# Optimization experiments

Measured on AMD Instinct MI355X. Metric: run time of the kernel, lower is better.

The kernel has to match this reference:

```python
import jax, jax.numpy as jnp
import numpy as np


def conv(x, w, b=None, pad=0):
    y = jax.lax.conv_general_dilated(x, w, (1, 1), [(pad, pad), (pad, pad)],
                                     dimension_numbers=('NCHW', 'OIHW', 'NCHW'))
    if b is not None:
        y = y + b[None, :, None, None]
    return y


def bn(x, g, b, m, v, eps=1e-5):
    scale = g / jnp.sqrt(v + eps)
    return (x - m[None, :, None, None]) * scale[None, :, None, None] + b[None, :, None, None]


def channel_gate(x, w1, b1, w2, b2):
    # avg pool -> MLP -> sigmoid, returns [B, C, 1, 1]
    p = x.mean(axis=(2, 3))                       # [B, C]
    h = jax.nn.relu(p @ w1.T + b1)                # [B, C//r]
    a = h @ w2.T + b2                             # [B, C]
    return jax.nn.sigmoid(a)[:, :, None, None]


def setup_inputs() -> dict:
    key = jax.random.key(0)
    ks = iter(jax.random.split(key, 48))
    B, Cin, H, W = 2, 256, 64, 64
    Ci = Cin // 2          # inter_channels = 128
    Cr = Ci // 16          # gate bottleneck = 8
    def nrm(shape, s=0.05):
        return jax.random.normal(next(ks), shape, jnp.float32) * s
    d = {}
    d['q'] = jax.random.normal(next(ks), (B, Cin, H, W), jnp.float32)
    d['s'] = jax.random.normal(next(ks), (B, Cin, H, W), jnp.float32)
    # Trans_s: conv3x3 + BN
    d['ts_w'] = nrm((Ci, Cin, 3, 3)); d['ts_b'] = jnp.zeros(Ci)
    d['ts_g'] = jnp.ones(Ci); d['ts_be'] = jnp.zeros(Ci)
    d['ts_m'] = nrm((Ci,), 0.01); d['ts_v'] = jnp.ones(Ci)
    # Trans_q: conv3x3 + BN
    d['tq_w'] = nrm((Ci, Cin, 3, 3)); d['tq_b'] = jnp.zeros(Ci)
    d['tq_g'] = jnp.ones(Ci); d['tq_be'] = jnp.zeros(Ci)
    d['tq_m'] = nrm((Ci,), 0.01); d['tq_v'] = jnp.ones(Ci)
    # common_v 1x1
    d['cv_w'] = nrm((Ci, Ci, 1, 1)); d['cv_b'] = jnp.zeros(Ci)
    # key/query 1x1 projections (out = Ci//2)
    d['k1_w'] = nrm((Ci // 2, Ci, 1, 1)); d['k1_b'] = jnp.zeros(Ci // 2)
    d['q1_w'] = nrm((Ci // 2, Ci, 1, 1)); d['q1_b'] = jnp.zeros(Ci // 2)
    d['k2_w'] = nrm((Ci // 2, Ci, 1, 1)); d['k2_b'] = jnp.zeros(Ci // 2)
    d['q2_w'] = nrm((Ci // 2, Ci, 1, 1)); d['q2_b'] = jnp.zeros(Ci // 2)
    # ChannelGate MLP
    d['g1_w'] = nrm((Cr, Ci)); d['g1_b'] = jnp.zeros(Cr)
    d['g2_w'] = nrm((Ci, Cr)); d['g2_b'] = jnp.zeros(Ci)
    # conv_cat: conv3x3 (no bias) + BN
    d['cc_w'] = nrm((Ci, 2 * Ci, 3, 3))
    d['cc_g'] = jnp.ones(Ci); d['cc_be'] = jnp.zeros(Ci)
    d['cc_m'] = nrm((Ci,), 0.01); d['cc_v'] = jnp.ones(Ci)
    return d


def reference(q, s, ts_w, ts_b, ts_g, ts_be, ts_m, ts_v,
              tq_w, tq_b, tq_g, tq_be, tq_m, tq_v,
              cv_w, cv_b, k1_w, k1_b, q1_w, q1_b, k2_w, k2_b, q2_w, q2_b,
              g1_w, g1_b, g2_w, g2_b, cc_w, cc_g, cc_be, cc_m, cc_v):
    # stems: conv3x3 + BN + ReLU
    s = jax.nn.relu(bn(conv(s, ts_w, ts_b, pad=1), ts_g, ts_be, ts_m, ts_v))
    q = jax.nn.relu(bn(conv(q, tq_w, tq_b, pad=1), tq_g, tq_be, tq_m, tq_v))
    B, C, H, W = q.shape
    N = H * W
    # values
    v_q1 = conv(q, cv_w, cv_b)                          # [B,C,H,W]
    v_s1 = conv(s, cv_w, cv_b)
    v_q = v_q1.reshape(B, C, N).transpose(0, 2, 1)      # [B,N,C]
    v_s = v_s1.reshape(B, C, N).transpose(0, 2, 1)
    # dual keys / queries with negation trick
    k1 = conv(s, k1_w, k1_b).reshape(B, C // 2, N)
    k2 = conv(q, k2_w, k2_b).reshape(B, C // 2, N)
    key_cat = jnp.concatenate([k1, -k2], axis=1).transpose(0, 2, 1)   # [B,N,C]
    q1x = conv(s, q1_w, q1_b).reshape(B, C // 2, N)
    q2x = conv(q, q2_w, q2_b).reshape(B, C // 2, N)
    query_cat = jnp.concatenate([q1x, q2x], axis=1)                    # [B,C,N]
    # abs-score attention, dual softmax from the same score matrix
    A_s = jnp.abs(jnp.einsum('bnc,bcm->bnm', key_cat, query_cat))      # [B,N,N]
    att_s = jax.nn.softmax(A_s, axis=-1)
    att_q = jax.nn.softmax(A_s.transpose(0, 2, 1), axis=-1)
    # attend + channel-gate SE fusion + residual
    p_s = jnp.einsum('bnm,bmc->bnc', att_s, v_s).transpose(0, 2, 1).reshape(B, C, H, W)
    E_s = channel_gate(v_s1, g1_w, g1_b, g2_w, g2_b) * p_s + s
    q_s = jnp.einsum('bnm,bmc->bnc', att_q, v_q).transpose(0, 2, 1).reshape(B, C, H, W)
    E_q = channel_gate(v_q1, g1_w, g1_b, g2_w, g2_b) * q_s + q
    # concat + conv3x3(no bias) + BN + ReLU
    cpam = jax.nn.relu(bn(conv(jnp.concatenate([E_q, E_s], axis=1), cc_w, None, pad=1),
                          cc_g, cc_be, cc_m, cc_v))
    return (cpam, E_q, E_s)
```

## Files before the change

kernel.cpp:

```cpp
#include <hip/hip_runtime.h>

typedef __bf16 bf16;
typedef __bf16 v8bf __attribute__((ext_vector_type(8)));
typedef __bf16 v4bf __attribute__((ext_vector_type(4)));
typedef float v4f __attribute__((ext_vector_type(4)));

#define MFMA16(a, b, c) __builtin_amdgcn_mfma_f32_16x16x32_bf16(a, b, c, 0, 0, 0)

__device__ __forceinline__ float sf(float x) {
  if (!(x == x)) return 0.f;
  return fminf(fmaxf(x, -1e30f), 1e30f);
}

__global__ __launch_bounds__(256) void fill_kernel(float* __restrict__ out, float v, int n) {
  int i = blockIdx.x * 256 + threadIdx.x;
  if (i < n) out[i] = v;
}

__global__ __launch_bounds__(256) void prep_kernel(
    const float* __restrict__ ts_w, const float* __restrict__ tq_w,
    const float* ts_b, const float* ts_g, const float* ts_be, const float* ts_m, const float* ts_v,
    const float* tq_b, const float* tq_g, const float* tq_be, const float* tq_m, const float* tq_v,
    bf16* __restrict__ Wt01, float* __restrict__ ss01)
{
  int idx = blockIdx.x * 256 + threadIdx.x;
  if (idx < 589824) {
    int which = idx / 294912;
    int rem = idx - which * 294912;
    int co = rem / 2304;
    int r2 = rem - co * 2304;
    int tap = r2 >> 8;
    int ci = r2 & 255;
    const float* W = which ? tq_w : ts_w;
    Wt01[idx] = (bf16)W[(co * 256 + ci) * 9 + tap];
  } else if (idx < 590080) {
    int i = idx - 589824;
    int which = i >> 7, c = i & 127;
    float g, be, m, vv, bias;
    if (which == 0) { g=ts_g[c]; be=ts_be[c]; m=ts_m[c]; vv=ts_v[c]; bias=ts_b[c]; }
    else            { g=tq_g[c]; be=tq_be[c]; m=tq_m[c]; vv=tq_v[c]; bias=tq_b[c]; }
    float scale = g / sqrtf(vv + 1e-5f);
    ss01[which * 256 + c] = sf(scale);
    ss01[which * 256 + 128 + c] = sf((bias - m) * scale + be);
  }
}

__global__ __launch_bounds__(256) void prep2_kernel(
    const float* __restrict__ cc_w, const float* cc_g, const float* cc_be,
    const float* cc_m, const float* cc_v,
    bf16* __restrict__ Wt2, float* __restrict__ ss_cc)
{
  int idx = blockIdx.x * 256 + threadIdx.x;
  if (idx < 294912) {
    int co = idx / 2304;
    int r2 = idx - co * 2304;
    int tap = r2 >> 8;
    int ci = r2 & 255;
    Wt2[idx] = (bf16)cc_w[(co * 256 + ci) * 9 + tap];
  } else if (idx < 295040) {
    int c = idx - 294912;
    float scale = cc_g[c] / sqrtf(cc_v[c] + 1e-5f);
    ss_cc[c] = sf(scale);
    ss_cc[128 + c] = sf(-cc_m[c] * scale + cc_be[c]);
  }
}

__global__ __launch_bounds__(256) void convN_kernel(
    const float* __restrict__ pS, const float* __restrict__ pQ,
    const bf16* __restrict__ Wb, const float* __restrict__ ssb,
    void* __restrict__ out_, int mode)
{
  __shared__ bf16 As[66][40];
  __shared__ bf16 Bs[3][64][40];

  int y = blockIdx.x;
  int co0 = blockIdx.y * 64;
  int z = blockIdx.z;
  int tsr = z >> 1, b = z & 1;

  const float *in0, *in1;
  const bf16* W;
  const float* sp;
  if (mode == 0) {
    const float* base = (tsr ? pQ : pS) + (long)b * 1048576;
    in0 = base; in1 = base + 524288;
    W = Wb + (long)tsr * 294912;
    sp = ssb + tsr * 256;
  } else {
    in0 = pS + 1048576 + (long)b * 524288;
    in1 = pS + 2097152 + (long)b * 524288;
    W = Wb; sp = ssb;
  }

  int t = threadIdx.x, lane = t & 63, w = t >> 6;
  int l15 = lane & 15, l4 = lane >> 4;
  int wr = (w & 1) * 32, wc = (w >> 1) * 32;
  int ac = t & 31, ag = t >> 5;
  int bco = t >> 2, bk = (t & 3) * 8;

  v4f acc[2][2] = {};

  auto loadA = [&](int it, v8bf& areg) {
    int dy = it >> 3, ks = it & 7;
    int ysrc = y + dy - 1;
    int cg = ks * 32 + ac;
    const float* ip = (cg < 128) ? (in0 + (long)cg * 4096) : (in1 + (long)(cg - 128) * 4096);
    if ((unsigned)ysrc < 64u) {
      const float* src = ip + ysrc * 64 + ag * 8;
#pragma unroll
      for (int i = 0; i < 8; ++i) areg[i] = (bf16)src[i];
    } else {
#pragma unroll
      for (int i = 0; i < 8; ++i) areg[i] = (bf16)0.f;
    }
  };
  auto loadB = [&](int it, v8bf* breg) {
    int dy = it >> 3, ks = it & 7;
    const bf16* wk = W + (long)(co0 + bco) * 2304 + dy * 3 * 256 + ks * 32 + bk;
#pragma unroll
    for (int d = 0; d < 3; ++d) breg[d] = *(const v8bf*)(wk + d * 256);
  };

  v8bf areg, breg[3];
  loadA(0, areg);
  loadB(0, breg);

  for (int it = 0; it < 24; ++it) {
    __syncthreads();
#pragma unroll
    for (int i = 0; i < 8; ++i) As[ag * 8 + 1 + i][ac] = areg[i];
    if (ag == 0) As[0][ac] = (bf16)0.f;
    if (ag == 7) As[65][ac] = (bf16)0.f;
#pragma unroll
    for (int d = 0; d < 3; ++d) *(v8bf*)&Bs[d][bco][bk] = breg[d];
    __syncthreads();
    if (it < 23) { loadA(it + 1, areg); loadB(it + 1, breg); }
#pragma unroll
    for (int d = 0; d < 3; ++d) {
      v8bf af0 = *(const v8bf*)&As[wr + d + l15][l4 * 8];
      v8bf af1 = *(const v8bf*)&As[wr + 16 + d + l15][l4 * 8];
#pragma unroll
      for (int j = 0; j < 2; ++j) {
        v8bf bfr = *(const v8bf*)&Bs[d][wc + j * 16 + l15][l4 * 8];
        acc[0][j] = MFMA16(af0, bfr, acc[0][j]);
        acc[1][j] = MFMA16(af1, bfr, acc[1][j]);
      }
    }
  }
#pragma unroll
  for (int i = 0; i < 2; ++i) {
    int nb = y * 64 + wr + i * 16 + l4 * 4;
#pragma unroll
    for (int j = 0; j < 2; ++j) {
      int c = co0 + wc + j * 16 + l15;
      float scale = sp[c], shift = sp[128 + c];
      if (mode == 0) {
        bf16* o = (bf16*)out_ + ((long)(tsr * 2 + b) * 4096 + nb) * 128 + c;
#pragma unroll
        for (int r = 0; r < 4; ++r)
          o[r * 128] = (bf16)sf(fmaxf(acc[i][j][r] * scale + shift, 0.f));
      } else {
        v4f pk;
#pragma unroll
        for (int r = 0; r < 4; ++r)
          pk[r] = sf(fmaxf(acc[i][j][r] * scale + shift, 0.f));
        *(v4f*)((float*)out_ + ((long)b * 128 + c) * 4096 + nb) = pk;
      }
    }
  }
}

__global__ __launch_bounds__(256) void conv1_kernel(
    const bf16* __restrict__ feat_base,
    const float* __restrict__ cv_w, const float* __restrict__ k1_w, const float* __restrict__ q1_w,
    const float* __restrict__ k2_w, const float* __restrict__ q2_w,
    const float* __restrict__ cv_b, const float* __restrict__ k1_b, const float* __restrict__ q1_b,
    const float* __restrict__ k2_b, const float* __restrict__ q2_b,
    bf16* __restrict__ v_base, bf16* __restrict__ keyT, bf16* __restrict__ queryT)
{
  int nt = blockIdx.x;
  int br = blockIdx.z >> 1, b = blockIdx.z & 1;
  long zid = br * 2 + b;
  const bf16* feat = feat_base + zid * 524288 + (long)nt * 4096;

  __shared__ bf16 As[32][40];
  __shared__ bf16 Bs[256][40];

  int t = threadIdx.x, lane = t & 63, w = t >> 6;
  int l15 = lane & 15, l4 = lane >> 4;
  int wr = (w & 1) * 16, wc = (w >> 1) * 128;

  const float* wrow;
  bool negk = false;
  if (t < 128)       wrow = cv_w + (long)t * 128;
  else if (t < 192) { wrow = (br ? k2_w : k1_w) + (long)(t - 128) * 128; negk = (br != 0); }
  else               wrow = (br ? q2_w : q1_w) + (long)(t - 192) * 128;

  v4f acc[8] = {};
  int ap = t >> 2, ak = (t & 3) * 8;

  for (int ks = 0; ks < 4; ++ks) {
    int ci0 = ks * 32;
    v8bf av;
    if (t < 128) av = *(const v8bf*)(feat + ap * 128 + ci0 + ak);
    float wv[32];
#pragma unroll
    for (int u = 0; u < 32; ++u) wv[u] = wrow[ci0 + u];
    if (negk) {
#pragma unroll
      for (int u = 0; u < 32; ++u) wv[u] = -wv[u];
    }
    __syncthreads();
    if (t < 128) *(v8bf*)&As[ap][ak] = av;
#pragma unroll
    for (int u = 0; u < 32; ++u) Bs[t][u] = (bf16)wv[u];
    __syncthreads();
    v8bf af = *(const v8bf*)&As[wr + l15][l4 * 8];
#pragma unroll
    for (int j = 0; j < 8; ++j) {
      v8bf bfr = *(const v8bf*)&Bs[wc + j * 16 + l15][l4 * 8];
      acc[j] = MFMA16(af, bfr, acc[j]);
    }
  }

  int nb = nt * 32 + wr + l4 * 4;
#pragma unroll
  for (int j = 0; j < 8; ++j) {
    int c = wc + j * 16 + l15;
    float bv;
    if (c < 128)      bv = cv_b[c];
    else if (c < 192) bv = br ? -k2_b[c - 128] : k1_b[c - 128];
    else              bv = (br ? q2_b : q1_b)[c - 192];
    float v0 = sf(acc[j][0] + bv), v1 = sf(acc[j][1] + bv);
    float v2 = sf(acc[j][2] + bv), v3 = sf(acc[j][3] + bv);
    if (c < 128) {
      v4bf pk;
      pk[0] = (bf16)v0; pk[1] = (bf16)v1; pk[2] = (bf16)v2; pk[3] = (bf16)v3;
      *(v4bf*)(v_base + zid * 524288 + (long)c * 4096 + nb) = pk;
    } else if (c < 192) {
      int cc = (c - 128) + br * 64;
      bf16* kp = keyT + (long)b * 524288 + (long)nb * 128 + cc;
      kp[0] = (bf16)v0; kp[128] = (bf16)v1; kp[256] = (bf16)v2; kp[384] = (bf16)v3;
    } else {
      int cc = (c - 192) + br * 64;
      bf16* qp = queryT + (long)b * 524288 + (long)nb * 128 + cc;
      qp[0] = (bf16)v0; qp[128] = (bf16)v1; qp[256] = (bf16)v2; qp[384] = (bf16)v3;
    }
  }
}

__global__ __launch_bounds__(64) void pmean_kernel(
    const bf16* __restrict__ vs, float* __restrict__ pmean)
{
  int c = blockIdx.x, z = blockIdx.y, l = threadIdx.x;
  const bf16* src = vs + ((long)z * 128 + c) * 4096;
  float s = 0.f;
#pragma unroll
  for (int k = 0; k < 8; ++k) {
    v8bf v = *(const v8bf*)(src + k * 512 + l * 8);
#pragma unroll
    for (int e = 0; e < 8; ++e) s += (float)v[e];
  }
  s += __shfl_xor(s, 1, 64);
  s += __shfl_xor(s, 2, 64);
  s += __shfl_xor(s, 4, 64);
  s += __shfl_xor(s, 8, 64);
  s += __shfl_xor(s, 16, 64);
  s += __shfl_xor(s, 32, 64);
  if (l == 0) pmean[z * 128 + c] = s * (1.f / 4096.f);
}

__global__ __launch_bounds__(128) void gate2_kernel(
    const float* __restrict__ pmean, const float* __restrict__ g1_w, const float* __restrict__ g1_b,
    const float* __restrict__ g2_w, const float* __restrict__ g2_b, float* __restrict__ gate)
{
  __shared__ float p[128];
  __shared__ float h[8];
  int z = blockIdx.x, t = threadIdx.x;
  p[t] = pmean[z * 128 + t];
  __syncthreads();
  if (t < 8) {
    float a = g1_b[t];
    for (int c = 0; c < 128; ++c) a += g1_w[t * 128 + c] * p[c];
    h[t] = fmaxf(a, 0.f);
  }
  __syncthreads();
  float a = g2_b[t];
#pragma unroll
  for (int j = 0; j < 8; ++j) a += g2_w[t * 8 + j] * h[j];
  gate[z * 128 + t] = sf(1.f / (1.f + __expf(-a)));
}

__global__ __launch_bounds__(256) void apply_kernel(
    const bf16* __restrict__ keyT, const bf16* __restrict__ queryT,
    const bf16* __restrict__ v_base, const float* __restrict__ gate,
    const bf16* __restrict__ feat_base, float* __restrict__ d_out)
{
  int nt = blockIdx.x, br = blockIdx.z >> 1, b = blockIdx.z & 1;
  int n0 = nt * 64;
  const bf16* X = (br ? queryT : keyT) + ((long)b * 4096 + n0) * 128;
  const bf16* Y = (br ? keyT : queryT) + (long)b * 4096 * 128;
  const bf16* V = v_base + (long)(br * 2 + b) * 524288;
  const float* gt = gate + (br * 2 + b) * 128;
  const bf16* feat = feat_base + (long)(br * 2 + b) * 524288 + (long)n0 * 128;

  __shared__ bf16 Ys[64][132];
  __shared__ bf16 Vs[128][68];
  __shared__ bf16 Ps[64][68];
  __shared__ float rps[4][64];

  int t = threadIdx.x, lane = t & 63, w = t >> 6;
  int l15 = lane & 15, l4 = lane >> 4;
  int wm = w * 16;
  int wr = (w & 1) * 32;
  int wc = (w >> 1) * 64;

#pragma unroll
  for (int i = 0; i < 4; ++i) {
    int ch = t + i * 256;
    *(v8bf*)&Ys[ch >> 4][(ch & 15) * 8] = *(const v8bf*)(X + (ch >> 4) * 128 + (ch & 15) * 8);
  }
  __syncthreads();
  v8bf af[4][4];
#pragma unroll
  for (int i = 0; i < 4; ++i)
#pragma unroll
    for (int k = 0; k < 4; ++k)
      af[i][k] = *(const v8bf*)&Ys[i * 16 + l15][k * 32 + l4 * 8];

  v4f acc[2][4] = {};
  float rp[4][4] = {};

  v8bf yreg[4], vreg[4];
#pragma unroll
  for (int i = 0; i < 4; ++i) {
    int ch = t + i * 256;
    yreg[i] = *(const v8bf*)(Y + (long)(ch >> 4) * 128 + (ch & 15) * 8);
    vreg[i] = *(const v8bf*)(V + (long)(ch >> 3) * 4096 + (ch & 7) * 8);
  }

  for (int mt = 0; mt < 64; ++mt) {
    __syncthreads();
#pragma unroll
    for (int i = 0; i < 4; ++i) {
      int ch = t + i * 256;
      *(v8bf*)&Ys[ch >> 4][(ch & 15) * 8] = yreg[i];
      *(v8bf*)&Vs[ch >> 3][(ch & 7) * 8] = vreg[i];
    }
    __syncthreads();
    if (mt < 63) {
      int m0 = (mt + 1) * 64;
#pragma unroll
      for (int i = 0; i < 4; ++i) {
        int ch = t + i * 256;
        yreg[i] = *(const v8bf*)(Y + (long)(m0 + (ch >> 4)) * 128 + (ch & 15) * 8);
        vreg[i] = *(const v8bf*)(V + (long)(ch >> 3) * 4096 + m0 + (ch & 7) * 8);
      }
    }
    v4f sacc[4] = {};
#pragma unroll
    for (int k = 0; k < 4; ++k) {
      v8bf by = *(const v8bf*)&Ys[wm + l15][k * 32 + l4 * 8];
#pragma unroll
      for (int i = 0; i < 4; ++i)
        sacc[i] = MFMA16(af[i][k], by, sacc[i]);
    }
#pragma unroll
    for (int i = 0; i < 4; ++i)
#pragma unroll
      for (int r = 0; r < 4; ++r) {
        float e = __expf(fminf(fabsf(sacc[i][r]), 80.f) - 50.f);
        rp[i][r] += e;
        Ps[i * 16 + l4 * 4 + r][wm + l15] = (bf16)e;
      }
    __syncthreads();
#pragma unroll
    for (int k = 0; k < 2; ++k) {
      v8bf p0 = *(const v8bf*)&Ps[wr + l15][k * 32 + l4 * 8];
      v8bf p1 = *(const v8bf*)&Ps[wr + 16 + l15][k * 32 + l4 * 8];
#pragma unroll
      for (int j = 0; j < 4; ++j) {
        v8bf vb = *(const v8bf*)&Vs[wc + j * 16 + l15][k * 32 + l4 * 8];
        acc[0][j] = MFMA16(p0, vb, acc[0][j]);
        acc[1][j] = MFMA16(p1, vb, acc[1][j]);
      }
    }
  }
#pragma unroll
  for (int i = 0; i < 4; ++i)
#pragma unroll
    for (int r = 0; r < 4; ++r) {
      float v = rp[i][r];
      v += __shfl_xor(v, 1, 64);
      v += __shfl_xor(v, 2, 64);
      v += __shfl_xor(v, 4, 64);
      v += __shfl_xor(v, 8, 64);
      if (l15 == 0) rps[w][i * 16 + l4 * 4 + r] = v;
    }
  __syncthreads();

  float* outE = d_out + (long)(br ? 1 : 2) * 1048576 + (long)b * 524288;
#pragma unroll
  for (int i = 0; i < 2; ++i) {
    int rowt = wr + i * 16 + l4 * 4;
    float dv[4];
#pragma unroll
    for (int r = 0; r < 4; ++r)
      dv[r] = fmaxf(rps[0][rowt + r] + rps[1][rowt + r] + rps[2][rowt + r] + rps[3][rowt + r],
                    1e-30f);
#pragma unroll
    for (int j = 0; j < 4; ++j) {
      int c = wc + j * 16 + l15;
      float g = gt[c];
      v4f pk;
#pragma unroll
      for (int r = 0; r < 4; ++r) {
        float val = acc[i][j][r] / dv[r] * g + (float)feat[(long)(rowt + r) * 128 + c];
        pk[r] = sf(val);
      }
      *(v4f*)(outE + (long)c * 4096 + n0 + rowt) = pk;
    }
  }
}

extern "C" void kernel_launch(void* const* d_in, const int* in_sizes, int n_in,
                              void* d_out, int out_size, void* d_ws, size_t ws_size,
                              hipStream_t stream)
{
  if (n_in != 33 || in_sizes[0] != 2097152 || in_sizes[2] != 294912 ||
      in_sizes[14] != 16384 || out_size != 3145728) {
    fill_kernel<<<12288, 256, 0, stream>>>((float*)d_out, 100.0f, 3145728);
    return;
  }
  if (ws_size < 12582912) {
    fill_kernel<<<12288, 256, 0, stream>>>((float*)d_out, 1.0f, 3145728);
    return;
  }

  const float* q_in = (const float*)d_in[0];
  const float* s_in = (const float*)d_in[1];
  char* ob = (char*)d_out;
  float* outf = (float*)d_out;

  float* gate  = (float*)(ob + 0);
  float* pmean = (float*)(ob + 2048);

  char* ws = (char*)d_ws;
  bf16*  sfeat  = (bf16*)(ws + 0);
  bf16*  vs     = (bf16*)(ws + 4194304);
  bf16*  keyT   = (bf16*)(ws + 8388608);
  bf16*  queryT = (bf16*)(ws + 10485760);
  bf16*  Wt01   = (bf16*)(ws + 8388608);
  float* ss01   = (float*)(ws + 10485760);
  bf16*  Wt2    = (bf16*)(ws + 0);
  float* ss_cc  = (float*)(ws + 589824);

  prep_kernel<<<2306, 256, 0, stream>>>(
      (const float*)d_in[2], (const float*)d_in[8],
      (const float*)d_in[3], (const float*)d_in[4], (const float*)d_in[5],
      (const float*)d_in[6], (const float*)d_in[7],
      (const float*)d_in[9], (const float*)d_in[10], (const float*)d_in[11],
      (const float*)d_in[12], (const float*)d_in[13],
      Wt01, ss01);

  convN_kernel<<<dim3(64, 2, 4), 256, 0, stream>>>(s_in, q_in, Wt01, ss01, sfeat, 0);

  conv1_kernel<<<dim3(128, 1, 4), 256, 0, stream>>>(
      sfeat,
      (const float*)d_in[14], (const float*)d_in[16], (const float*)d_in[18],
      (const float*)d_in[20], (const float*)d_in[22],
      (const float*)d_in[15], (const float*)d_in[17], (const float*)d_in[19],
      (const float*)d_in[21], (const float*)d_in[23],
      vs, keyT, queryT);

  pmean_kernel<<<dim3(128, 4), 64, 0, stream>>>(vs, pmean);

  gate2_kernel<<<4, 128, 0, stream>>>(pmean, (const float*)d_in[24], (const float*)d_in[25],
                                      (const float*)d_in[26], (const float*)d_in[27], gate);

  apply_kernel<<<dim3(64, 1, 4), 256, 0, stream>>>(keyT, queryT, vs, gate, sfeat, outf);

  prep2_kernel<<<1153, 256, 0, stream>>>(
      (const float*)d_in[28], (const float*)d_in[29], (const float*)d_in[30],
      (const float*)d_in[31], (const float*)d_in[32], Wt2, ss_cc);

  convN_kernel<<<dim3(64, 2, 2), 256, 0, stream>>>(outf, nullptr, Wt2, ss_cc, outf, 1);
}
```

Baseline: 300.3 us.

## Read MFMA operands directly from global memory and double-buffer LDS tiles

The conv kernel no longer stages weights in LDS. Each lane loads its B fragment straight from global memory, and the A tile is double-buffered so one barrier per iteration suffices. The attention apply kernel drops the Ys/Vs LDS staging and register prefetch, reading X, Y and V fragments directly from global (relying on L1/L2), and double-buffers the P tile. The weight prep kernels now have each thread handle one (co,ci) pair and loop over the 9 taps, so far fewer threads are launched. This removes LDS traffic and barriers but gives up explicit prefetch overlap, so global latency is exposed in the MFMA loops.

```diff
diff --git a/kernel.cpp b/kernel.cpp
--- a/kernel.cpp
+++ b/kernel.cpp
@@ -24,17 +24,16 @@
     bf16* __restrict__ Wt01, float* __restrict__ ss01)
 {
   int idx = blockIdx.x * 256 + threadIdx.x;
-  if (idx < 589824) {
-    int which = idx / 294912;
-    int rem = idx - which * 294912;
-    int co = rem / 2304;
-    int r2 = rem - co * 2304;
-    int tap = r2 >> 8;
-    int ci = r2 & 255;
-    const float* W = which ? tq_w : ts_w;
-    Wt01[idx] = (bf16)W[(co * 256 + ci) * 9 + tap];
-  } else if (idx < 590080) {
-    int i = idx - 589824;
+  if (idx < 65536) {
+    int which = idx >> 15;
+    int rem = idx & 32767;
+    int co = rem >> 8, ci = rem & 255;
+    const float* src = (which ? tq_w : ts_w) + (long)(co * 256 + ci) * 9;
+    bf16* dst = Wt01 + which * 294912 + co * 2304 + ci;
+#pragma unroll
+    for (int tap = 0; tap < 9; ++tap) dst[tap * 256] = (bf16)src[tap];
+  } else if (idx < 65792) {
+    int i = idx - 65536;
     int which = i >> 7, c = i & 127;
     float g, be, m, vv, bias;
     if (which == 0) { g=ts_g[c]; be=ts_be[c]; m=ts_m[c]; vv=ts_v[c]; bias=ts_b[c]; }
@@ -51,14 +50,14 @@
     bf16* __restrict__ Wt2, float* __restrict__ ss_cc)
 {
   int idx = blockIdx.x * 256 + threadIdx.x;
-  if (idx < 294912) {
-    int co = idx / 2304;
-    int r2 = idx - co * 2304;
-    int tap = r2 >> 8;
-    int ci = r2 & 255;
-    Wt2[idx] = (bf16)cc_w[(co * 256 + ci) * 9 + tap];
-  } else if (idx < 295040) {
-    int c = idx - 294912;
+  if (idx < 32768) {
+    int co = idx >> 8, ci = idx & 255;
+    const float* src = cc_w + (long)(co * 256 + ci) * 9;
+    bf16* dst = Wt2 + co * 2304 + ci;
+#pragma unroll
+    for (int tap = 0; tap < 9; ++tap) dst[tap * 256] = (bf16)src[tap];
+  } else if (idx < 32896) {
+    int c = idx - 32768;
     float scale = cc_g[c] / sqrtf(cc_v[c] + 1e-5f);
     ss_cc[c] = sf(scale);
     ss_cc[128 + c] = sf(-cc_m[c] * scale + cc_be[c]);
@@ -70,8 +69,7 @@
     const bf16* __restrict__ Wb, const float* __restrict__ ssb,
     void* __restrict__ out_, int mode)
 {
-  __shared__ bf16 As[66][40];
-  __shared__ bf16 Bs[3][64][40];
+  __shared__ bf16 As[2][66][40];
 
   int y = blockIdx.x;
   int co0 = blockIdx.y * 64;
@@ -96,7 +94,6 @@
   int l15 = lane & 15, l4 = lane >> 4;
   int wr = (w & 1) * 32, wc = (w >> 1) * 32;
   int ac = t & 31, ag = t >> 5;
-  int bco = t >> 2, bk = (t & 3) * 8;
 
   v4f acc[2][2] = {};
 
@@ -114,34 +111,27 @@
       for (int i = 0; i < 8; ++i) areg[i] = (bf16)0.f;
     }
   };
-  auto loadB = [&](int it, v8bf* breg) {
+
+  v8bf areg;
+  loadA(0, areg);
+
+  for (int it = 0; it < 24; ++it) {
+    int buf = it & 1;
     int dy = it >> 3, ks = it & 7;
-    const bf16* wk = W + (long)(co0 + bco) * 2304 + dy * 3 * 256 + ks * 32 + bk;
-#pragma unroll
-    for (int d = 0; d < 3; ++d) breg[d] = *(const v8bf*)(wk + d * 256);
-  };
-
-  v8bf areg, breg[3];
-  loadA(0, areg);
-  loadB(0, breg);
-
-  for (int it = 0; it < 24; ++it) {
+#pragma unroll
+    for (int i = 0; i < 8; ++i) As[buf][ag * 8 + 1 + i][ac] = areg[i];
+    if (ag == 0) As[buf][0][ac] = (bf16)0.f;
+    if (ag == 7) As[buf][65][ac] = (bf16)0.f;
     __syncthreads();
-#pragma unroll
-    for (int i = 0; i < 8; ++i) As[ag * 8 + 1 + i][ac] = areg[i];
-    if (ag == 0) As[0][ac] = (bf16)0.f;
-    if (ag == 7) As[65][ac] = (bf16)0.f;
-#pragma unroll
-    for (int d = 0; d < 3; ++d) *(v8bf*)&Bs[d][bco][bk] = breg[d];
-    __syncthreads();
-    if (it < 23) { loadA(it + 1, areg); loadB(it + 1, breg); }
+    if (it < 23) loadA(it + 1, areg);
 #pragma unroll
     for (int d = 0; d < 3; ++d) {
-      v8bf af0 = *(const v8bf*)&As[wr + d + l15][l4 * 8];
-      v8bf af1 = *(const v8bf*)&As[wr + 16 + d + l15][l4 * 8];
+      v8bf af0 = *(const v8bf*)&As[buf][wr + d + l15][l4 * 8];
+      v8bf af1 = *(const v8bf*)&As[buf][wr + 16 + d + l15][l4 * 8];
 #pragma unroll
       for (int j = 0; j < 2; ++j) {
-        v8bf bfr = *(const v8bf*)&Bs[d][wc + j * 16 + l15][l4 * 8];
+        v8bf bfr = *(const v8bf*)(W + (long)(co0 + wc + j * 16 + l15) * 2304 +
+                                  (dy * 3 + d) * 256 + ks * 32 + l4 * 8);
         acc[0][j] = MFMA16(af0, bfr, acc[0][j]);
         acc[1][j] = MFMA16(af1, bfr, acc[1][j]);
       }
@@ -304,9 +294,7 @@
   const float* gt = gate + (br * 2 + b) * 128;
   const bf16* feat = feat_base + (long)(br * 2 + b) * 524288 + (long)n0 * 128;
 
-  __shared__ bf16 Ys[64][132];
-  __shared__ bf16 Vs[128][68];
-  __shared__ bf16 Ps[64][68];
+  __shared__ bf16 Ps[2][64][68];
   __shared__ float rps[4][64];
 
   int t = threadIdx.x, lane = t & 63, w = t >> 6;
@@ -315,52 +303,24 @@
   int wr = (w & 1) * 32;
   int wc = (w >> 1) * 64;
 
-#pragma unroll
-  for (int i = 0; i < 4; ++i) {
-    int ch = t + i * 256;
-    *(v8bf*)&Ys[ch >> 4][(ch & 15) * 8] = *(const v8bf*)(X + (ch >> 4) * 128 + (ch & 15) * 8);
-  }
-  __syncthreads();
   v8bf af[4][4];
 #pragma unroll
   for (int i = 0; i < 4; ++i)
 #pragma unroll
     for (int k = 0; k < 4; ++k)
-      af[i][k] = *(const v8bf*)&Ys[i * 16 + l15][k * 32 + l4 * 8];
+      af[i][k] = *(const v8bf*)(X + (i * 16 + l15) * 128 + k * 32 + l4 * 8);
 
   v4f acc[2][4] = {};
   float rp[4][4] = {};
 
-  v8bf yreg[4], vreg[4];
-#pragma unroll
-  for (int i = 0; i < 4; ++i) {
-    int ch = t + i * 256;
-    yreg[i] = *(const v8bf*)(Y + (long)(ch >> 4) * 128 + (ch & 15) * 8);
-    vreg[i] = *(const v8bf*)(V + (long)(ch >> 3) * 4096 + (ch & 7) * 8);
-  }
-
   for (int mt = 0; mt < 64; ++mt) {
-    __syncthreads();
-#pragma unroll
-    for (int i = 0; i < 4; ++i) {
-      int ch = t + i * 256;
-      *(v8bf*)&Ys[ch >> 4][(ch & 15) * 8] = yreg[i];
-      *(v8bf*)&Vs[ch >> 3][(ch & 7) * 8] = vreg[i];
-    }
-    __syncthreads();
-    if (mt < 63) {
-      int m0 = (mt + 1) * 64;
-#pragma unroll
-      for (int i = 0; i < 4; ++i) {
-        int ch = t + i * 256;
-        yreg[i] = *(const v8bf*)(Y + (long)(m0 + (ch >> 4)) * 128 + (ch & 15) * 8);
-        vreg[i] = *(const v8bf*)(V + (long)(ch >> 3) * 4096 + m0 + (ch & 7) * 8);
-      }
-    }
+    int m0 = mt * 64;
+    int buf = mt & 1;
+    const bf16* yp = Y + (long)(m0 + wm + l15) * 128 + l4 * 8;
     v4f sacc[4] = {};
 #pragma unroll
     for (int k = 0; k < 4; ++k) {
-      v8bf by = *(const v8bf*)&Ys[wm + l15][k * 32 + l4 * 8];
+      v8bf by = *(const v8bf*)(yp + k * 32);
 #pragma unroll
       for (int i = 0; i < 4; ++i)
         sacc[i] = MFMA16(af[i][k], by, sacc[i]);
@@ -371,16 +331,17 @@
       for (int r = 0; r < 4; ++r) {
         float e = __expf(fminf(fabsf(sacc[i][r]), 80.f) - 50.f);
         rp[i][r] += e;
-        Ps[i * 16 + l4 * 4 + r][wm + l15] = (bf16)e;
+        Ps[buf][i * 16 + l4 * 4 + r][wm + l15] = (bf16)e;
       }
     __syncthreads();
+    const bf16* vp = V + m0 + l4 * 8;
 #pragma unroll
     for (int k = 0; k < 2; ++k) {
-      v8bf p0 = *(const v8bf*)&Ps[wr + l15][k * 32 + l4 * 8];
-      v8bf p1 = *(const v8bf*)&Ps[wr + 16 + l15][k * 32 + l4 * 8];
+      v8bf p0 = *(const v8bf*)&Ps[buf][wr + l15][k * 32 + l4 * 8];
+      v8bf p1 = *(const v8bf*)&Ps[buf][wr + 16 + l15][k * 32 + l4 * 8];
 #pragma unroll
       for (int j = 0; j < 4; ++j) {
-        v8bf vb = *(const v8bf*)&Vs[wc + j * 16 + l15][k * 32 + l4 * 8];
+        v8bf vb = *(const v8bf*)(vp + (long)(wc + j * 16 + l15) * 4096 + k * 32);
         acc[0][j] = MFMA16(p0, vb, acc[0][j]);
         acc[1][j] = MFMA16(p1, vb, acc[1][j]);
       }
@@ -455,7 +416,7 @@
   bf16*  Wt2    = (bf16*)(ws + 0);
   float* ss_cc  = (float*)(ws + 589824);
 
-  prep_kernel<<<2306, 256, 0, stream>>>(
+  prep_kernel<<<258, 256, 0, stream>>>(
       (const float*)d_in[2], (const float*)d_in[8],
       (const float*)d_in[3], (const float*)d_in[4], (const float*)d_in[5],
       (const float*)d_in[6], (const float*)d_in[7],
@@ -480,7 +441,7 @@
 
   apply_kernel<<<dim3(64, 1, 4), 256, 0, stream>>>(keyT, queryT, vs, gate, sfeat, outf);
 
-  prep2_kernel<<<1153, 256, 0, stream>>>(
+  prep2_kernel<<<129, 256, 0, stream>>>(
       (const float*)d_in[28], (const float*)d_in[29], (const float*)d_in[30],
       (const float*)d_in[31], (const float*)d_in[32], Wt2, ss_cc);
 
```

Result: slower. 381.3 us (+27.0%).
